# Performance work log

Measured on AMD Instinct MI355X. Metric: run time of the kernel, lower is better.

## Reference

```python
import jax, jax.numpy as jnp
import numpy as np

N_NODES = 100000
N_EDGES = 400000
N_GRAPHS = 5000
IN, H, OUT = 11, 256, 1


def setup_inputs() -> dict:
    key = jax.random.key(0)
    ks = jax.random.split(key, 16)

    def xav(k, shape):
        fan_in, fan_out = shape[-2], shape[-1]
        std = float(np.sqrt(2.0 / (fan_in + fan_out)))
        return jax.random.normal(k, shape, dtype=jnp.float32) * std

    x = jax.random.normal(ks[0], (N_NODES, IN), dtype=jnp.float32)
    edge_index = jax.random.randint(ks[1], (2, N_EDGES), 0, N_NODES, dtype=jnp.int64)
    batch = jnp.sort(jax.random.randint(ks[2], (N_NODES,), 0, N_GRAPHS, dtype=jnp.int64))
    return {
        "x": x,
        "edge_index": edge_index,
        "batch": batch,
        "gin0_w1": xav(ks[3], (IN, H)),
        "gin0_b1": jnp.zeros((H,), jnp.float32),
        "gin0_w2": xav(ks[4], (H, H)),
        "gin0_b2": jnp.zeros((H,), jnp.float32),
        "gin_w1": xav(ks[5], (4, H, H)),
        "gin_b1": jnp.zeros((4, H), jnp.float32),
        "gin_w2": xav(ks[6], (4, H, H)),
        "gin_b2": jnp.zeros((4, H), jnp.float32),
        "head_w1": xav(ks[7], (H, H)),
        "head_b1": jnp.zeros((H,), jnp.float32),
        "head_w2": xav(ks[8], (H, OUT)),
        "head_b2": jnp.zeros((OUT,), jnp.float32),
    }


def _gin(x, src, dst, w1, b1, w2, b2):
    # GINConv (eps=0): MLP(x + sum_{j->i} x_j), then outer ReLU from forward()
    agg = jax.ops.segment_sum(x[src], dst, num_segments=N_NODES)
    h = x + agg
    h = jnp.matmul(jax.nn.relu(jnp.matmul(h, w1) + b1), w2) + b2
    return jax.nn.relu(h)  # dropout p=0.15 is identity in eval


def reference(x, edge_index, batch, gin0_w1, gin0_b1, gin0_w2, gin0_b2,
              gin_w1, gin_b1, gin_w2, gin_b2,
              head_w1, head_b1, head_w2, head_b2):
    src, dst = edge_index[0], edge_index[1]
    h = _gin(x, src, dst, gin0_w1, gin0_b1, gin0_w2, gin0_b2)
    for i in range(4):
        h = _gin(h, src, dst, gin_w1[i], gin_b1[i], gin_w2[i], gin_b2[i])
    # global mean pool over graphs
    sums = jax.ops.segment_sum(h, batch, num_segments=N_GRAPHS)
    cnts = jax.ops.segment_sum(jnp.ones((h.shape[0],), h.dtype), batch, num_segments=N_GRAPHS)
    pooled = sums / jnp.maximum(cnts, 1.0)[:, None]
    # head: Linear -> Dropout(0.25, identity in eval) -> Linear
    out = jnp.matmul(pooled, head_w1) + head_b1
    out = jnp.matmul(out, head_w2) + head_b2
    return out
```

## Files before the change

### kernel.cpp

```cpp
#include <hip/hip_runtime.h>
#include <hip/hip_bf16.h>


constexpr int HDIM = 256;

typedef short v8s __attribute__((ext_vector_type(8)));
typedef float v4f __attribute__((ext_vector_type(4)));

__device__ __forceinline__ float bflo(unsigned int u) { return __uint_as_float(u << 16); }
__device__ __forceinline__ float bfhi(unsigned int u) { return __uint_as_float(u & 0xffff0000u); }
__device__ __forceinline__ unsigned short f2bf(float f) {
    unsigned int u = __float_as_uint(f);
    return (unsigned short)((u + 0x7fffu + ((u >> 16) & 1u)) >> 16);
}

__device__ __forceinline__ void gload16(const void* g, void* l) {
    __builtin_amdgcn_global_load_lds(
        (const __attribute__((address_space(1))) unsigned int*)g,
        (__attribute__((address_space(3))) unsigned int*)l, 16, 0, 0);
}

__global__ __launch_bounds__(256) void hist_kernel(
    const int* __restrict__ dst, int* __restrict__ deg, int n_edges)
{
    int e = blockIdx.x * 256 + threadIdx.x;
    if (e < n_edges) atomicAdd(&deg[dst[e]], 1);
}

__global__ __launch_bounds__(256) void scan1_kernel(
    const int* __restrict__ deg, int* __restrict__ scanex,
    int* __restrict__ partials, int n)
{
    __shared__ int s[256];
    int i = blockIdx.x * 256 + threadIdx.x;
    int v = (i < n) ? deg[i] : 0;
    s[threadIdx.x] = v;
    __syncthreads();
#pragma unroll
    for (int off = 1; off < 256; off <<= 1) {
        int t = (threadIdx.x >= off) ? s[threadIdx.x - off] : 0;
        __syncthreads();
        s[threadIdx.x] += t;
        __syncthreads();
    }
    if (i < n) scanex[i] = s[threadIdx.x] - v;
    if (threadIdx.x == 255) partials[blockIdx.x] = s[255];
}

__global__ __launch_bounds__(512) void scan2_kernel(int* __restrict__ partials, int nb)
{
    __shared__ int s[512];
    int v = (threadIdx.x < nb) ? partials[threadIdx.x] : 0;
    s[threadIdx.x] = v;
    __syncthreads();
#pragma unroll
    for (int off = 1; off < 512; off <<= 1) {
        int t = (threadIdx.x >= off) ? s[threadIdx.x - off] : 0;
        __syncthreads();
        s[threadIdx.x] += t;
        __syncthreads();
    }
    if (threadIdx.x < nb) partials[threadIdx.x] = s[threadIdx.x] - v;
}

__global__ __launch_bounds__(256) void scan3_kernel(
    const int* __restrict__ scanex, const int* __restrict__ partials,
    int* __restrict__ rowptr, int* __restrict__ cursor, int n, int n_edges)
{
    int i = blockIdx.x * 256 + threadIdx.x;
    if (i < n) {
        int v = scanex[i] + partials[blockIdx.x];
        rowptr[i] = v;
        cursor[i] = v;
    }
    if (i == 0) rowptr[n] = n_edges;
}

__global__ __launch_bounds__(256) void fill_kernel(
    const int* __restrict__ src, const int* __restrict__ dst,
    int* __restrict__ cursor, int* __restrict__ csr_src, int n_edges)
{
    int e = blockIdx.x * 256 + threadIdx.x;
    if (e >= n_edges) return;
    int slot = atomicAdd(&cursor[dst[e]], 1);
    csr_src[slot] = src[e];
}

__global__ __launch_bounds__(256) void convw_kernel(
    const float* __restrict__ g0w2, const float* __restrict__ gw1,
    const float* __restrict__ gw2, unsigned short* __restrict__ Bts)
{
    int gid = blockIdx.x * 256 + threadIdx.x;
    if (gid >= 9 * 65536) return;
    int m = gid >> 16;
    int e = gid & 0xffff;
    int n = e >> 8, k = e & 255;
    const float* W = (m == 0) ? g0w2
                   : (m <= 4) ? gw1 + (size_t)(m - 1) * 65536
                              : gw2 + (size_t)(m - 5) * 65536;
    Bts[(size_t)m * 65536 + n * 256 + k] = f2bf(W[k * 256 + n]);
}

__global__ __launch_bounds__(256) void agg0_kernel(
    const float* __restrict__ x, const int* __restrict__ rowptr,
    const int* __restrict__ csr_src, float* __restrict__ xsum, int n)
{
    int gid = blockIdx.x * 256 + threadIdx.x;
    int node = gid >> 4, f = gid & 15;
    if (node >= n || f >= 11) return;
    float acc = x[(size_t)node * 11 + f];
    int beg = rowptr[node], end = rowptr[node + 1];
    for (int e = beg; e < end; e++)
        acc += x[(size_t)csr_src[e] * 11 + f];
    xsum[(size_t)node * 11 + f] = acc;
}

__global__ __launch_bounds__(256) void agg_bf_kernel(
    const unsigned short* __restrict__ h, const int* __restrict__ rowptr,
    const int* __restrict__ csr_src, unsigned short* __restrict__ out, int n)
{
    int node = blockIdx.x * 4 + (threadIdx.x >> 6);
    if (node >= n) return;
    int lane = threadIdx.x & 63;
    uint2 raw = *(const uint2*)&h[(size_t)node * HDIM + lane * 4];
    float a0 = bflo(raw.x), a1 = bfhi(raw.x), a2 = bflo(raw.y), a3 = bfhi(raw.y);
    int beg = rowptr[node], end = rowptr[node + 1];
    for (int e = beg; e < end; e++) {
        int s = csr_src[e];
        uint2 r = *(const uint2*)&h[(size_t)s * HDIM + lane * 4];
        a0 += bflo(r.x); a1 += bfhi(r.x); a2 += bflo(r.y); a3 += bfhi(r.y);
    }
    uint2 o;
    o.x = (unsigned int)f2bf(a0) | ((unsigned int)f2bf(a1) << 16);
    o.y = (unsigned int)f2bf(a2) | ((unsigned int)f2bf(a3) << 16);
    *(uint2*)&out[(size_t)node * HDIM + lane * 4] = o;
}

__global__ __launch_bounds__(256) void gemm0_kernel(
    const float* __restrict__ xsum, const float* __restrict__ w1,
    const float* __restrict__ b1, unsigned short* __restrict__ out, int M)
{
    int row = blockIdx.x * 4 + (threadIdx.x >> 6);
    if (row >= M) return;
    int lane = threadIdx.x & 63;
    float xr[11];
#pragma unroll
    for (int k = 0; k < 11; k++) xr[k] = xsum[(size_t)row * 11 + k];
    int n = lane * 4;
    float4 acc = *(const float4*)&b1[n];
#pragma unroll
    for (int k = 0; k < 11; k++) {
        float4 w = *(const float4*)&w1[k * HDIM + n];
        acc.x = fmaf(xr[k], w.x, acc.x);
        acc.y = fmaf(xr[k], w.y, acc.y);
        acc.z = fmaf(xr[k], w.z, acc.z);
        acc.w = fmaf(xr[k], w.w, acc.w);
    }
    uint2 o;
    o.x = (unsigned int)f2bf(fmaxf(acc.x, 0.f)) | ((unsigned int)f2bf(fmaxf(acc.y, 0.f)) << 16);
    o.y = (unsigned int)f2bf(fmaxf(acc.z, 0.f)) | ((unsigned int)f2bf(fmaxf(acc.w, 0.f)) << 16);
    *(uint2*)&out[(size_t)row * HDIM + n] = o;
}

__global__ __launch_bounds__(256) void gemm_mfma(
    const unsigned short* __restrict__ A, const unsigned short* __restrict__ Wt,
    const float* __restrict__ bias, unsigned short* __restrict__ C,
    int M, int do_relu)
{
    __shared__ short lds[2][512 * 8];
    const int tid = threadIdx.x;
    const int w = tid >> 6, lane = tid & 63;
    const int q = lane >> 4, r = lane & 15;
    const int rh = w & 1, ch = w >> 1;
    const int m0 = blockIdx.x * 128, n0 = blockIdx.y * 128;

    v4f acc[4][4];
#pragma unroll
    for (int i = 0; i < 4; i++)
#pragma unroll
        for (int j = 0; j < 4; j++)
            acc[i][j] = (v4f){0.f, 0.f, 0.f, 0.f};

    for (int kt = 0; kt < HDIM; kt += 32) {
#pragma unroll
        for (int rd = 0; rd < 2; rd++) {
            int cb = rd * 256 + w * 64;
            int s  = cb + lane;
            int row = s >> 2;
            int ko  = ((s & 3) - (row >> 1)) & 3;
            int gr = m0 + row; if (gr >= M) gr = M - 1;
            gload16(&A[(size_t)gr * HDIM + kt + ko * 8],  &lds[0][cb * 8]);
            gload16(&Wt[(size_t)(n0 + row) * HDIM + kt + ko * 8], &lds[1][cb * 8]);
        }
        __syncthreads();
        v8s af[4], bf[4];
#pragma unroll
        for (int mi = 0; mi < 4; mi++) {
            int row = rh * 64 + mi * 16 + r;
            int slot = row * 4 + ((q + (row >> 1)) & 3);
            af[mi] = *(const v8s*)&lds[0][slot * 8];
        }
#pragma unroll
        for (int ni = 0; ni < 4; ni++) {
            int row = ch * 64 + ni * 16 + r;
            int slot = row * 4 + ((q + (row >> 1)) & 3);
            bf[ni] = *(const v8s*)&lds[1][slot * 8];
        }
#pragma unroll
        for (int mi = 0; mi < 4; mi++)
#pragma unroll
            for (int ni = 0; ni < 4; ni++)
                acc[mi][ni] = __builtin_amdgcn_mfma_f32_16x16x32_bf16(
                    af[mi], bf[ni], acc[mi][ni], 0, 0, 0);
        __syncthreads();
    }

    float bv[4];
#pragma unroll
    for (int ni = 0; ni < 4; ni++)
        bv[ni] = bias[n0 + ch * 64 + ni * 16 + r];

    short* cw = &lds[0][0] + w * (16 * 72);
#pragma unroll
    for (int mi = 0; mi < 4; mi++) {
#pragma unroll
        for (int ni = 0; ni < 4; ni++)
#pragma unroll
            for (int i = 0; i < 4; i++) {
                float v = acc[mi][ni][i] + bv[ni];
                if (do_relu) v = fmaxf(v, 0.f);
                cw[(q * 4 + i) * 72 + ni * 16 + r] = (short)f2bf(v);
            }
        __syncthreads();
        int row = lane >> 2, seg = lane & 3;
        int gm = m0 + rh * 64 + mi * 16 + row;
        if (gm < M) {
            v8s p0 = *(const v8s*)&cw[row * 72 + seg * 16];
            v8s p1 = *(const v8s*)&cw[row * 72 + seg * 16 + 8];
            size_t o = (size_t)gm * HDIM + n0 + ch * 64 + seg * 16;
            *(v8s*)&C[o]     = p0;
            *(v8s*)&C[o + 8] = p1;
        }
        __syncthreads();
    }
}

__global__ __launch_bounds__(256) void gemm_head(
    const float* __restrict__ A, const float* __restrict__ B,
    const float* __restrict__ bias, float* __restrict__ C, int M)
{
    __shared__ float As[16][132];
    __shared__ float Bs[16][132];
    const int tid = threadIdx.x;
    const int tx = tid & 15, ty = tid >> 4;
    const int m0 = blockIdx.x * 128, n0 = blockIdx.y * 128;
    const int arow = tid >> 1, acs = (tid & 1) * 8;
    int gr = m0 + arow; if (gr >= M) gr = M - 1;
    float acc[8][8] = {};

    for (int kt = 0; kt < HDIM; kt += 16) {
        float f[8];
        *(float4*)&f[0] = *(const float4*)&A[(size_t)gr * HDIM + kt + acs];
        *(float4*)&f[4] = *(const float4*)&A[(size_t)gr * HDIM + kt + acs + 4];
#pragma unroll
        for (int j = 0; j < 8; j++) As[acs + j][arow] = f[j];
#pragma unroll
        for (int i = 0; i < 2; i++) {
            int lid = tid * 2 + i;
            int kr = lid >> 5, ns = (lid & 31) * 4;
            *(float4*)&Bs[kr][ns] =
                *(const float4*)&B[(size_t)(kt + kr) * HDIM + n0 + ns];
        }
        __syncthreads();
#pragma unroll
        for (int kl = 0; kl < 16; kl++) {
            float a[8], b[8];
            *(float4*)&a[0] = *(const float4*)&As[kl][ty * 8];
            *(float4*)&a[4] = *(const float4*)&As[kl][ty * 8 + 4];
            *(float4*)&b[0] = *(const float4*)&Bs[kl][tx * 8];
            *(float4*)&b[4] = *(const float4*)&Bs[kl][tx * 8 + 4];
#pragma unroll
            for (int i = 0; i < 8; i++)
#pragma unroll
                for (int j = 0; j < 8; j++)
                    acc[i][j] = fmaf(a[i], b[j], acc[i][j]);
        }
        __syncthreads();
    }

    float bv[8];
    *(float4*)&bv[0] = *(const float4*)&bias[n0 + tx * 8];
    *(float4*)&bv[4] = *(const float4*)&bias[n0 + tx * 8 + 4];
#pragma unroll
    for (int i = 0; i < 8; i++) {
        int gr2 = m0 + ty * 8 + i;
        if (gr2 >= M) break;
        float o[8];
#pragma unroll
        for (int j = 0; j < 8; j++) o[j] = acc[i][j] + bv[j];
        *(float4*)&C[(size_t)gr2 * HDIM + n0 + tx * 8]     = *(float4*)&o[0];
        *(float4*)&C[(size_t)gr2 * HDIM + n0 + tx * 8 + 4] = *(float4*)&o[4];
    }
}

__global__ __launch_bounds__(256) void bounds_kernel(
    const int* __restrict__ batch, int* __restrict__ gstart, int n, int ngraphs)
{
    int i = blockIdx.x * 256 + threadIdx.x;
    if (i >= n) return;
    int b1 = batch[i];
    int b0 = (i == 0) ? -1 : batch[i - 1];
    for (int g = b0 + 1; g <= b1; g++) gstart[g] = i;
    if (i == n - 1)
        for (int g = b1 + 1; g <= ngraphs; g++) gstart[g] = n;
}

__global__ __launch_bounds__(256) void pool_kernel(
    const unsigned short* __restrict__ h, const int* __restrict__ gstart,
    float* __restrict__ pooled, int ngraphs)
{
    int g = blockIdx.x * 4 + (threadIdx.x >> 6);
    if (g >= ngraphs) return;
    int lane = threadIdx.x & 63;
    int beg = gstart[g], end = gstart[g + 1];
    float a0 = 0.f, a1 = 0.f, a2 = 0.f, a3 = 0.f;
    for (int i = beg; i < end; i++) {
        uint2 r = *(const uint2*)&h[(size_t)i * HDIM + lane * 4];
        a0 += bflo(r.x); a1 += bfhi(r.x); a2 += bflo(r.y); a3 += bfhi(r.y);
    }
    float inv = 1.0f / fmaxf((float)(end - beg), 1.0f);
    float4 o = { a0 * inv, a1 * inv, a2 * inv, a3 * inv };
    *(float4*)&pooled[(size_t)g * HDIM + lane * 4] = o;
}

__global__ __launch_bounds__(256) void head2_kernel(
    const float* __restrict__ hh, const float* __restrict__ w2,
    const float* __restrict__ b2, float* __restrict__ out, int n_graphs)
{
    int g = blockIdx.x * 4 + (threadIdx.x >> 6);
    int lane = threadIdx.x & 63;
    float p = 0.f;
    if (g < n_graphs) {
        float4 v = *(const float4*)&hh[(size_t)g * HDIM + lane * 4];
        float4 w = *(const float4*)&w2[lane * 4];
        p = v.x * w.x + v.y * w.y + v.z * w.z + v.w * w.w;
    }
#pragma unroll
    for (int off = 32; off > 0; off >>= 1) p += __shfl_down(p, off, 64);
    if (g < n_graphs && lane == 0) out[g] = p + b2[0];
}

extern "C" void kernel_launch(void* const* d_in, const int* in_sizes, int n_in,
                              void* d_out, int out_size, void* d_ws, size_t ws_size,
                              hipStream_t stream)
{
    const float* x    = (const float*)d_in[0];
    const int*   ei   = (const int*)d_in[1];
    const int*   batch= (const int*)d_in[2];
    const float* g0w1 = (const float*)d_in[3];
    const float* g0b1 = (const float*)d_in[4];
    const float* g0w2 = (const float*)d_in[5];
    const float* g0b2 = (const float*)d_in[6];
    const float* gw1  = (const float*)d_in[7];
    const float* gb1  = (const float*)d_in[8];
    const float* gw2  = (const float*)d_in[9];
    const float* gb2  = (const float*)d_in[10];
    const float* hw1  = (const float*)d_in[11];
    const float* hb1  = (const float*)d_in[12];
    const float* hw2  = (const float*)d_in[13];
    const float* hb2  = (const float*)d_in[14];

    const int n_nodes  = in_sizes[0] / 11;
    const int n_edges  = in_sizes[1] / 2;
    const int n_graphs = out_size;

    const int* srcp = ei;
    const int* dstp = ei + n_edges;

    const size_t NF = (size_t)n_nodes * HDIM;
    char* p = (char*)d_ws;
    unsigned short* H0 = (unsigned short*)p; p += NF * 2;
    unsigned short* H1 = (unsigned short*)p; p += NF * 2;
    unsigned short* H2 = (unsigned short*)p; p += NF * 2;
    unsigned short* Bts = (unsigned short*)p; p += (size_t)9 * 65536 * 2;
    float* xsum    = (float*)p; p += (size_t)n_nodes * 11 * 4;
    float* pooled  = (float*)p; p += (size_t)n_graphs * HDIM * 4;
    float* hh      = (float*)p; p += (size_t)n_graphs * HDIM * 4;
    int* deg       = (int*)p; p += (size_t)n_nodes * 4;
    int* scanex    = (int*)p; p += (size_t)n_nodes * 4;
    int* partials  = (int*)p; p += 512 * 4;
    int* rowptr    = (int*)p; p += ((size_t)n_nodes + 1) * 4;
    int* cursor    = (int*)p; p += (size_t)n_nodes * 4;
    int* csr_src   = (int*)p; p += (size_t)n_edges * 4;
    int* gstart    = (int*)p; p += ((size_t)n_graphs + 1) * 4;
    if ((size_t)(p - (char*)d_ws) > ws_size) return;

    const int nblk = (n_nodes + 255) / 256;

    convw_kernel<<<(9 * 65536 + 255) / 256, 256, 0, stream>>>(g0w2, gw1, gw2, Bts);

    hipMemsetAsync(deg, 0, (size_t)n_nodes * 4, stream);
    hist_kernel<<<(n_edges + 255) / 256, 256, 0, stream>>>(dstp, deg, n_edges);
    scan1_kernel<<<nblk, 256, 0, stream>>>(deg, scanex, partials, n_nodes);
    scan2_kernel<<<1, 512, 0, stream>>>(partials, nblk);
    scan3_kernel<<<nblk, 256, 0, stream>>>(scanex, partials, rowptr, cursor,
                                           n_nodes, n_edges);
    fill_kernel<<<(n_edges + 255) / 256, 256, 0, stream>>>(
        srcp, dstp, cursor, csr_src, n_edges);

    bounds_kernel<<<nblk, 256, 0, stream>>>(batch, gstart, n_nodes, n_graphs);

    const int gemmGridX = (n_nodes + 127) / 128;
    const int aggGrid   = (n_nodes + 3) / 4;

    agg0_kernel<<<((size_t)n_nodes * 16 + 255) / 256, 256, 0, stream>>>(
        x, rowptr, csr_src, xsum, n_nodes);
    gemm0_kernel<<<aggGrid, 256, 0, stream>>>(xsum, g0w1, g0b1, H1, n_nodes);
    gemm_mfma<<<dim3(gemmGridX, 2), 256, 0, stream>>>(
        H1, Bts + 0, g0b2, H0, n_nodes, 1);

    unsigned short* cur = H0;
    unsigned short* t   = H1;
    unsigned short* y   = H2;
    for (int l = 0; l < 4; l++) {
        const float* b1 = gb1 + (size_t)l * HDIM;
        const float* b2 = gb2 + (size_t)l * HDIM;
        agg_bf_kernel<<<aggGrid, 256, 0, stream>>>(cur, rowptr, csr_src, t, n_nodes);
        gemm_mfma<<<dim3(gemmGridX, 2), 256, 0, stream>>>(
            t, Bts + (size_t)(1 + l) * 65536, b1, y, n_nodes, 1);
        gemm_mfma<<<dim3(gemmGridX, 2), 256, 0, stream>>>(
            y, Bts + (size_t)(5 + l) * 65536, b2, t, n_nodes, 1);
        unsigned short* dead = cur;
        cur = t; t = dead;
    }

    pool_kernel<<<(n_graphs + 3) / 4, 256, 0, stream>>>(cur, gstart, pooled, n_graphs);

    gemm_head<<<dim3((n_graphs + 127) / 128, 2), 256, 0, stream>>>(
        pooled, hw1, hb1, hh, n_graphs);
    head2_kernel<<<(n_graphs + 3) / 4, 256, 0, stream>>>(
        hh, hw2, hb2, (float*)d_out, n_graphs);
}
```

Before: 789.6 us.

## Fuse GIN layer's two GEMMs into one kernel and widen aggregation loads

Adds mlp_fused, which computes both MLP linears of a GIN layer for a 64-row tile. The ReLU'd intermediate is kept in LDS as bf16 instead of being written to and reread from global memory, which removes the H2 buffer and one kernel launch per layer. The aggregation kernel now uses 32 lanes per node with 16-byte loads, covering 8 nodes per block. In exchange, each block reloads the full W1 and W2 weights per 64-row tile without double buffering, LDS use rises to about 52KB, and the grid has more, smaller tiles.

```diff
diff --git a/kernel.cpp b/kernel.cpp
--- a/kernel.cpp
+++ b/kernel.cpp
@@ -119,21 +119,25 @@
     const unsigned short* __restrict__ h, const int* __restrict__ rowptr,
     const int* __restrict__ csr_src, unsigned short* __restrict__ out, int n)
 {
-    int node = blockIdx.x * 4 + (threadIdx.x >> 6);
+    int node = blockIdx.x * 8 + (threadIdx.x >> 5);
     if (node >= n) return;
-    int lane = threadIdx.x & 63;
-    uint2 raw = *(const uint2*)&h[(size_t)node * HDIM + lane * 4];
+    int l = threadIdx.x & 31;
+    uint4 raw = *(const uint4*)&h[(size_t)node * HDIM + l * 8];
     float a0 = bflo(raw.x), a1 = bfhi(raw.x), a2 = bflo(raw.y), a3 = bfhi(raw.y);
+    float a4 = bflo(raw.z), a5 = bfhi(raw.z), a6 = bflo(raw.w), a7 = bfhi(raw.w);
     int beg = rowptr[node], end = rowptr[node + 1];
     for (int e = beg; e < end; e++) {
         int s = csr_src[e];
-        uint2 r = *(const uint2*)&h[(size_t)s * HDIM + lane * 4];
+        uint4 r = *(const uint4*)&h[(size_t)s * HDIM + l * 8];
         a0 += bflo(r.x); a1 += bfhi(r.x); a2 += bflo(r.y); a3 += bfhi(r.y);
-    }
-    uint2 o;
+        a4 += bflo(r.z); a5 += bfhi(r.z); a6 += bflo(r.w); a7 += bfhi(r.w);
+    }
+    uint4 o;
     o.x = (unsigned int)f2bf(a0) | ((unsigned int)f2bf(a1) << 16);
     o.y = (unsigned int)f2bf(a2) | ((unsigned int)f2bf(a3) << 16);
-    *(uint2*)&out[(size_t)node * HDIM + lane * 4] = o;
+    o.z = (unsigned int)f2bf(a4) | ((unsigned int)f2bf(a5) << 16);
+    o.w = (unsigned int)f2bf(a6) | ((unsigned int)f2bf(a7) << 16);
+    *(uint4*)&out[(size_t)node * HDIM + l * 8] = o;
 }
 
 __global__ __launch_bounds__(256) void gemm0_kernel(
@@ -238,6 +242,157 @@
             v8s p0 = *(const v8s*)&cw[row * 72 + seg * 16];
             v8s p1 = *(const v8s*)&cw[row * 72 + seg * 16 + 8];
             size_t o = (size_t)gm * HDIM + n0 + ch * 64 + seg * 16;
+            *(v8s*)&C[o]     = p0;
+            *(v8s*)&C[o + 8] = p1;
+        }
+        __syncthreads();
+    }
+}
+
+__global__ __launch_bounds__(256) void mlp_fused(
+    const unsigned short* __restrict__ A,
+    const unsigned short* __restrict__ W1t, const float* __restrict__ b1,
+    const unsigned short* __restrict__ W2t, const float* __restrict__ b2,
+    unsigned short* __restrict__ C, int M)
+{
+    __shared__ short Ybuf[8 * 2048];
+    __shared__ short Astage[256 * 8];
+    __shared__ short Wstage[1024 * 8];
+    const int tid = threadIdx.x;
+    const int w = tid >> 6, lane = tid & 63;
+    const int q = lane >> 4, r = lane & 15;
+    const int m0 = blockIdx.x * 64;
+
+    v4f acc[4][4];
+#pragma unroll
+    for (int i = 0; i < 4; i++)
+#pragma unroll
+        for (int j = 0; j < 4; j++)
+            acc[i][j] = (v4f){0.f, 0.f, 0.f, 0.f};
+
+    for (int kc = 0; kc < 8; kc++) {
+        int kt = kc * 32;
+        {
+            int s = tid;
+            int row = s >> 2;
+            int ko = ((s & 3) - (row >> 1)) & 3;
+            int gr = m0 + row; if (gr >= M) gr = M - 1;
+            gload16(&A[(size_t)gr * HDIM + kt + ko * 8], &Astage[(w * 64) * 8]);
+        }
+#pragma unroll
+        for (int rd = 0; rd < 4; rd++) {
+            int cb = rd * 256 + w * 64;
+            int s = cb + lane;
+            int n = s >> 2;
+            int ko = ((s & 3) - (n >> 1)) & 3;
+            gload16(&W1t[(size_t)n * HDIM + kt + ko * 8], &Wstage[cb * 8]);
+        }
+        __syncthreads();
+        v8s af[4], bf[4];
+#pragma unroll
+        for (int mi = 0; mi < 4; mi++) {
+            int row = mi * 16 + r;
+            int slot = row * 4 + ((q + (row >> 1)) & 3);
+            af[mi] = *(const v8s*)&Astage[slot * 8];
+        }
+#pragma unroll
+        for (int ni = 0; ni < 4; ni++) {
+            int n = w * 64 + ni * 16 + r;
+            int slot = n * 4 + ((q + (n >> 1)) & 3);
+            bf[ni] = *(const v8s*)&Wstage[slot * 8];
+        }
+#pragma unroll
+        for (int mi = 0; mi < 4; mi++)
+#pragma unroll
+            for (int ni = 0; ni < 4; ni++)
+                acc[mi][ni] = __builtin_amdgcn_mfma_f32_16x16x32_bf16(
+                    af[mi], bf[ni], acc[mi][ni], 0, 0, 0);
+        __syncthreads();
+    }
+
+    {
+        float bv1[4];
+#pragma unroll
+        for (int ni = 0; ni < 4; ni++)
+            bv1[ni] = b1[w * 64 + ni * 16 + r];
+#pragma unroll
+        for (int mi = 0; mi < 4; mi++)
+#pragma unroll
+            for (int ni = 0; ni < 4; ni++)
+#pragma unroll
+                for (int i = 0; i < 4; i++) {
+                    float v = fmaxf(acc[mi][ni][i] + bv1[ni], 0.f);
+                    int row = mi * 16 + q * 4 + i;
+                    int col = w * 64 + ni * 16 + r;
+                    int chunk = col >> 5, kk = col & 31;
+                    int ko = kk >> 3, j = kk & 7;
+                    int slot = row * 4 + ((ko + (row >> 1)) & 3);
+                    Ybuf[chunk * 2048 + slot * 8 + j] = (short)f2bf(v);
+                }
+    }
+    __syncthreads();
+
+    v4f acc2[4][4];
+#pragma unroll
+    for (int i = 0; i < 4; i++)
+#pragma unroll
+        for (int j = 0; j < 4; j++)
+            acc2[i][j] = (v4f){0.f, 0.f, 0.f, 0.f};
+
+    for (int kc = 0; kc < 8; kc++) {
+        int kt = kc * 32;
+#pragma unroll
+        for (int rd = 0; rd < 4; rd++) {
+            int cb = rd * 256 + w * 64;
+            int s = cb + lane;
+            int n = s >> 2;
+            int ko = ((s & 3) - (n >> 1)) & 3;
+            gload16(&W2t[(size_t)n * HDIM + kt + ko * 8], &Wstage[cb * 8]);
+        }
+        __syncthreads();
+        v8s af[4], bf[4];
+#pragma unroll
+        for (int mi = 0; mi < 4; mi++) {
+            int row = mi * 16 + r;
+            int slot = row * 4 + ((q + (row >> 1)) & 3);
+            af[mi] = *(const v8s*)&Ybuf[kc * 2048 + slot * 8];
+        }
+#pragma unroll
+        for (int ni = 0; ni < 4; ni++) {
+            int n = w * 64 + ni * 16 + r;
+            int slot = n * 4 + ((q + (n >> 1)) & 3);
+            bf[ni] = *(const v8s*)&Wstage[slot * 8];
+        }
+#pragma unroll
+        for (int mi = 0; mi < 4; mi++)
+#pragma unroll
+            for (int ni = 0; ni < 4; ni++)
+                acc2[mi][ni] = __builtin_amdgcn_mfma_f32_16x16x32_bf16(
+                    af[mi], bf[ni], acc2[mi][ni], 0, 0, 0);
+        __syncthreads();
+    }
+
+    float bv2[4];
+#pragma unroll
+    for (int ni = 0; ni < 4; ni++)
+        bv2[ni] = b2[w * 64 + ni * 16 + r];
+    short* cw = &Ybuf[w * 1152];
+#pragma unroll
+    for (int mi = 0; mi < 4; mi++) {
+#pragma unroll
+        for (int ni = 0; ni < 4; ni++)
+#pragma unroll
+            for (int i = 0; i < 4; i++) {
+                float v = fmaxf(acc2[mi][ni][i] + bv2[ni], 0.f);
+                cw[(q * 4 + i) * 72 + ni * 16 + r] = (short)f2bf(v);
+            }
+        __syncthreads();
+        int row = lane >> 2, seg = lane & 3;
+        int gm = m0 + mi * 16 + row;
+        if (gm < M) {
+            v8s p0 = *(const v8s*)&cw[row * 72 + seg * 16];
+            v8s p1 = *(const v8s*)&cw[row * 72 + seg * 16 + 8];
+            size_t o = (size_t)gm * HDIM + w * 64 + seg * 16;
             *(v8s*)&C[o]     = p0;
             *(v8s*)&C[o + 8] = p1;
         }
@@ -381,7 +536,6 @@
     char* p = (char*)d_ws;
     unsigned short* H0 = (unsigned short*)p; p += NF * 2;
     unsigned short* H1 = (unsigned short*)p; p += NF * 2;
-    unsigned short* H2 = (unsigned short*)p; p += NF * 2;
     unsigned short* Bts = (unsigned short*)p; p += (size_t)9 * 65536 * 2;
     float* xsum    = (float*)p; p += (size_t)n_nodes * 11 * 4;
     float* pooled  = (float*)p; p += (size_t)n_graphs * HDIM * 4;
@@ -410,28 +564,22 @@
 
     bounds_kernel<<<nblk, 256, 0, stream>>>(batch, gstart, n_nodes, n_graphs);
 
-    const int gemmGridX = (n_nodes + 127) / 128;
-    const int aggGrid   = (n_nodes + 3) / 4;
-
     agg0_kernel<<<((size_t)n_nodes * 16 + 255) / 256, 256, 0, stream>>>(
         x, rowptr, csr_src, xsum, n_nodes);
-    gemm0_kernel<<<aggGrid, 256, 0, stream>>>(xsum, g0w1, g0b1, H1, n_nodes);
-    gemm_mfma<<<dim3(gemmGridX, 2), 256, 0, stream>>>(
+    gemm0_kernel<<<(n_nodes + 3) / 4, 256, 0, stream>>>(xsum, g0w1, g0b1, H1, n_nodes);
+    gemm_mfma<<<dim3((n_nodes + 127) / 128, 2), 256, 0, stream>>>(
         H1, Bts + 0, g0b2, H0, n_nodes, 1);
 
     unsigned short* cur = H0;
     unsigned short* t   = H1;
-    unsigned short* y   = H2;
+    const int aggGrid = (n_nodes + 7) / 8;
+    const int mlpGrid = (n_nodes + 63) / 64;
     for (int l = 0; l < 4; l++) {
-        const float* b1 = gb1 + (size_t)l * HDIM;
-        const float* b2 = gb2 + (size_t)l * HDIM;
         agg_bf_kernel<<<aggGrid, 256, 0, stream>>>(cur, rowptr, csr_src, t, n_nodes);
-        gemm_mfma<<<dim3(gemmGridX, 2), 256, 0, stream>>>(
-            t, Bts + (size_t)(1 + l) * 65536, b1, y, n_nodes, 1);
-        gemm_mfma<<<dim3(gemmGridX, 2), 256, 0, stream>>>(
-            y, Bts + (size_t)(5 + l) * 65536, b2, t, n_nodes, 1);
-        unsigned short* dead = cur;
-        cur = t; t = dead;
+        mlp_fused<<<mlpGrid, 256, 0, stream>>>(
+            t, Bts + (size_t)(1 + l) * 65536, gb1 + (size_t)l * HDIM,
+            Bts + (size_t)(5 + l) * 65536, gb2 + (size_t)l * HDIM,
+            cur, n_nodes);
     }
 
     pool_kernel<<<(n_graphs + 3) / 4, 256, 0, stream>>>(cur, gstart, pooled, n_graphs);
```

Measured after the change: 665.2 us. 15.7% less time.
